# Optimization experiments

Measured on AMD Instinct MI355X. Metric: run time of the kernel, lower is better.

Reference implementation:

```python
import jax, jax.numpy as jnp
import numpy as np

NUM_HEADS = 12
NUM_GROUPS = 4
METRIC_SCALE = 1.0
CLS_MIX = 1.0
MEAN_MIX = 0.5
ROUTER_SCALE = 1.0
DIFF_SCALE = 1.0
B, N, D, HF = 16, 577, 768, 3072


def _ln(x, g, b, eps=1e-5):
    mu = jnp.mean(x, axis=-1, keepdims=True)
    var = jnp.mean(jnp.square(x - mu), axis=-1, keepdims=True)
    return (x - mu) * jax.lax.rsqrt(var + eps) * g + b


def setup_inputs() -> dict:
    key = jax.random.key(0)
    ks = iter(jax.random.split(key, 16))
    w = lambda shape, std: jax.random.normal(next(ks), shape, jnp.float32) * std
    return {
        "x": w((B, N, D), 1.0),
        "ln1_g": jnp.ones((D,)), "ln1_b": jnp.zeros((D,)),
        "ad_ln_g": jnp.ones((D,)), "ad_ln_b": jnp.zeros((D,)),
        "ad_w": w((D, D), 0.02),
        "w_qkv": w((D, 3 * D), 0.02),
        "w_proj": w((D, D), 0.02), "b_proj": jnp.zeros((D,)),
        "ln2_g": jnp.ones((D,)), "ln2_b": jnp.zeros((D,)),
        "fc1_w": w((D, HF), 0.02), "fc1_b": jnp.zeros((HF,)),
        "fc2_w": w((HF, D), 0.02), "fc2_b": jnp.zeros((D,)),
        "r_ln_g": jnp.ones((HF,)), "r_ln_b": jnp.zeros((HF,)),
        "r_proj_w": w((2 * HF, NUM_GROUPS), 0.02), "r_proj_b": jnp.zeros((NUM_GROUPS,)),
        "r_gate_w": w((2 * HF, 1), 0.02), "r_gate_b": jnp.full((1,), -2.0),
        "r_scale": jnp.full((NUM_GROUPS,), 0.1),
        "d_ln_g": jnp.ones((HF,)), "d_ln_b": jnp.zeros((HF,)),
        "d_out_w": w((HF, HF), 0.005),
        "d_gate_w": w((HF, 1), 0.02), "d_gate_b": jnp.full((1,), -1.5),
    }


def reference(x, ln1_g, ln1_b, ad_ln_g, ad_ln_b, ad_w, w_qkv, w_proj, b_proj,
              ln2_g, ln2_b, fc1_w, fc1_b, fc2_w, fc2_b,
              r_ln_g, r_ln_b, r_proj_w, r_proj_b, r_gate_w, r_gate_b, r_scale,
              d_ln_g, d_ln_b, d_out_w, d_gate_w, d_gate_b):
    b, n, d = x.shape
    hd = d // NUM_HEADS
    # ---- GeoAttention (pre-norm) ----
    h = _ln(x, ln1_g, ln1_b)
    # metric adapter: residual LN+Linear (SharedAttentionMetricAdapter)
    metric_h = h + METRIC_SCALE * (_ln(h, ad_ln_g, ad_ln_b) @ ad_w)
    # q,k from metric path; v from plain path (asymmetric Q/K vs V)
    qk = metric_h @ w_qkv[:, : 2 * d]                # [b,n,2d]
    v = h @ w_qkv[:, 2 * d :]                        # [b,n,d]
    q = qk[..., :d].reshape(b, n, NUM_HEADS, hd).transpose(0, 2, 1, 3)
    k = qk[..., d:].reshape(b, n, NUM_HEADS, hd).transpose(0, 2, 1, 3)
    v = v.reshape(b, n, NUM_HEADS, hd).transpose(0, 2, 1, 3)
    attn = jax.nn.softmax(jnp.einsum("bhnd,bhmd->bhnm", q, k) * (hd ** -0.5), axis=-1)
    out = jnp.einsum("bhnm,bhmd->bhnd", attn, v).transpose(0, 2, 1, 3).reshape(b, n, d)
    x = x + out @ w_proj + b_proj
    # ---- GeoMlp (pre-norm) ----
    h2 = _ln(x, ln2_g, ln2_b)
    hid = h2 @ fc1_w + fc1_b                         # [b,n,HF]
    # GroupCompetitionRouter on hidden
    rn = _ln(hid, r_ln_g, r_ln_b)
    summary = jnp.concatenate([CLS_MIX * rn[:, 0], MEAN_MIX * jnp.mean(rn[:, 1:], axis=1)], axis=-1)  # [b,2HF]
    wts = jax.nn.softmax(summary @ r_proj_w + r_proj_b, axis=-1)       # [b,G]
    gate = jax.nn.sigmoid(summary @ r_gate_w + r_gate_b)               # [b,1]
    centered = wts * float(NUM_GROUPS) - 1.0
    grouped = hid.reshape(b, n, NUM_GROUPS, HF // NUM_GROUPS)
    scale = 1.0 + ROUTER_SCALE * gate[:, None, :, None] * r_scale[None, None, :, None] * centered[:, None, :, None]
    hid = (grouped * scale).reshape(b, n, HF)
    # TokenDiffusionMixer on hidden
    dn = _ln(hid, d_ln_g, d_ln_b)
    tr = dn / jnp.maximum(jnp.linalg.norm(dn, axis=-1, keepdims=True), 1e-12)
    aff = jax.nn.softmax(jnp.einsum("bnc,bmc->bnm", tr, tr) * (HF ** -0.5), axis=-1)
    diffusion = jnp.einsum("bnm,bmc->bnc", aff, dn) - dn
    dgate = jax.nn.sigmoid(dn[:, 0] @ d_gate_w + d_gate_b)             # [b,1]
    hid = hid + DIFF_SCALE * dgate[:, :, None] * (diffusion @ d_out_w)
    # activation + fc2
    hid = jax.nn.gelu(hid, approximate=False)
    return x + hid @ fc2_w + fc2_b
```

## Files before the change

kernel.cpp:

```cpp
#include <hip/hip_runtime.h>
#include <math.h>

typedef unsigned short u16;
typedef unsigned int   u32;
typedef __attribute__((ext_vector_type(4))) float f32x4;
typedef __attribute__((ext_vector_type(4))) u32   u32x4;

#define DEV __device__ __forceinline__
#define AS1 __attribute__((address_space(1)))
#define AS3 __attribute__((address_space(3)))

DEV float b2f(u16 u){ u32 x = ((u32)u)<<16; float f; __builtin_memcpy(&f,&x,4); return f; }
DEV u16 f2b(float f){ u32 x; __builtin_memcpy(&x,&f,4); u32 r = x + 0x7FFFu + ((x>>16)&1u); return (u16)(r>>16); }

DEV float ldf(const float* p, long i){ return p[i]; }
DEV float ldf(const u16*   p, long i){ return b2f(p[i]); }

DEV void gload16(const u16* g, u16* l){
  __builtin_amdgcn_global_load_lds((const AS1 u32*)(const void*)g,
                                   (AS3 u32*)(void*)l, 16, 0, 0);
}

DEV float wave_sum(float v){
#pragma unroll
  for(int o=32;o;o>>=1) v += __shfl_down(v,o,64);
  return v;
}
DEV float wave_max(float v){
#pragma unroll
  for(int o=32;o;o>>=1) v = fmaxf(v, __shfl_down(v,o,64));
  return v;
}
DEV float block_sum(float v, float* tmp){
  v = wave_sum(v);
  if((threadIdx.x&63)==0) tmp[threadIdx.x>>6]=v;
  __syncthreads();
  float r = tmp[0]+tmp[1]+tmp[2]+tmp[3];
  __syncthreads();
  return r;
}
DEV float block_max(float v, float* tmp){
  v = wave_max(v);
  if((threadIdx.x&63)==0) tmp[threadIdx.x>>6]=v;
  __syncthreads();
  float r = fmaxf(fmaxf(tmp[0],tmp[1]),fmaxf(tmp[2],tmp[3]));
  __syncthreads();
  return r;
}

template<typename TI>
__global__ void transpose_pad(const TI* __restrict__ in, u16* __restrict__ out,
                              int R, int C, int Rpad, long strideI, long strideO){
  __shared__ u16 t[32][33];
  in  += (long)blockIdx.z*strideI;
  out += (long)blockIdx.z*strideO;
  int tx = threadIdx.x & 31, ty = threadIdx.x >> 5;
  int bc = blockIdx.x*32, br = blockIdx.y*32;
#pragma unroll
  for(int i=0;i<32;i+=8){
    int r = br+ty+i, c = bc+tx;
    float v = (r<R && c<C) ? ldf(in,(long)r*C+c) : 0.f;
    t[ty+i][tx] = f2b(v);
  }
  __syncthreads();
#pragma unroll
  for(int i=0;i<32;i+=8){
    int c = bc+ty+i, r = br+tx;
    if(c<C && r<Rpad) out[(long)c*Rpad + r] = t[tx][ty+i];
  }
}

template<typename TI>
__global__ void ln_rows(const TI* __restrict__ x, const float* __restrict__ g,
                        const float* __restrict__ b, u16* __restrict__ y, int W){
  __shared__ float tmp[4];
  long base=(long)blockIdx.x*W;
  float s=0.f, ss=0.f;
  for(int c=threadIdx.x;c<W;c+=256){ float v=ldf(x,base+c); s+=v; ss+=v*v; }
  s=block_sum(s,tmp); ss=block_sum(ss,tmp);
  float mu=s/W;
  float rstd=rsqrtf(fmaxf(ss/W-mu*mu,0.f)+1e-5f);
  for(int c=threadIdx.x;c<W;c+=256){
    float v=ldf(x,base+c);
    y[base+c]=f2b((v-mu)*rstd*g[c]+b[c]);
  }
}

__global__ void row_stats(const u16* __restrict__ x, float* __restrict__ stats, int W){
  __shared__ float tmp[4];
  long base=(long)blockIdx.x*W;
  float s=0.f,ss=0.f;
  for(int c=threadIdx.x;c<W;c+=256){ float v=b2f(x[base+c]); s+=v; ss+=v*v; }
  s=block_sum(s,tmp); ss=block_sum(ss,tmp);
  if(threadIdx.x==0){
    float mu=s/W;
    stats[2*(long)blockIdx.x]=mu;
    stats[2*(long)blockIdx.x+1]=rsqrtf(fmaxf(ss/W-mu*mu,0.f)+1e-5f);
  }
}

__global__ void dn_kernel(const u16* __restrict__ x, const float* __restrict__ g,
                          const float* __restrict__ b, const float* __restrict__ scalef,
                          u16* __restrict__ dn, float* __restrict__ rn){
  const int W=3072;
  __shared__ float tmp[4];
  __shared__ u16 rowb[3072];
  long row=(long)blockIdx.x;
  long base=row*(long)W;
  int bz=(int)(row/577);
  float s=0.f,ss=0.f;
  for(int c=threadIdx.x;c<W;c+=256){
    float sc=scalef[bz*4 + ((c>>8)/3)];
    float v=b2f(x[base+c])*sc;
    rowb[c]=f2b(v);
    s+=v; ss+=v*v;
  }
  s=block_sum(s,tmp); ss=block_sum(ss,tmp);
  float mu=s/W;
  float rstd=rsqrtf(fmaxf(ss/W-mu*mu,0.f)+1e-5f);
  float sq=0.f;
  for(int c=threadIdx.x;c<W;c+=256){
    float v=(b2f(rowb[c])-mu)*rstd*g[c]+b[c];
    sq+=v*v;
  }
  sq=block_sum(sq,tmp);
  float r=1.f/fmaxf(sqrtf(sq),1e-12f);
  for(int c=threadIdx.x;c<W;c+=256){
    float v=(b2f(rowb[c])-mu)*rstd*g[c]+b[c];
    dn[base+c]=f2b(v);
  }
  if(threadIdx.x==0) rn[blockIdx.x]=r;
}

__global__ void softmax_rows(u16* __restrict__ S, int W, int Wp,
                             const float* __restrict__ rs, int rpb, float alpha){
  __shared__ float tmp[4];
  long row = blockIdx.x;
  u16* p = S + row*(long)Wp;
  float rowscale = alpha;
  const float* rsb = nullptr;
  if(rs){ long bt=row/rpb; int m=(int)(row%rpb); rsb = rs + bt*(long)rpb; rowscale *= rsb[m]; }
  float mx=-3e38f;
  for(int c=threadIdx.x;c<W;c+=256){
    float v=b2f(p[c])*rowscale; if(rs) v*=rsb[c];
    mx=fmaxf(mx,v);
  }
  mx=block_max(mx,tmp);
  float sm=0.f;
  for(int c=threadIdx.x;c<W;c+=256){
    float v=b2f(p[c])*rowscale; if(rs) v*=rsb[c];
    sm+=__expf(v-mx);
  }
  sm=block_sum(sm,tmp);
  float inv=1.f/sm;
  for(int c=threadIdx.x;c<W;c+=256){
    float v=b2f(p[c])*rowscale; if(rs) v*=rsb[c];
    p[c]=f2b(__expf(v-mx)*inv);
  }
  for(int c=W+threadIdx.x;c<Wp;c+=256) p[c]=0;
}

__global__ void split_heads(const u16* __restrict__ qk, u16* __restrict__ qh, u16* __restrict__ kh){
  int i = blockIdx.x*256+threadIdx.x;
  if(i >= 16*577*12*8) return;
  int dv = i&7; int h=(i>>3)%12; int bn=i/96;
  int b=bn/577, n=bn%577;
  long src=(long)bn*1536 + h*64 + dv*8;
  long dst=((long)((b*12+h)*577+n))*64 + dv*8;
  *(u32x4*)(qh+dst) = *(const u32x4*)(qk+src);
  *(u32x4*)(kh+dst) = *(const u32x4*)(qk+src+768);
}
__global__ void merge_heads(const u16* __restrict__ aoh, u16* __restrict__ aout){
  int i = blockIdx.x*256+threadIdx.x;
  if(i >= 16*577*12*8) return;
  int dv=i&7; int h=(i>>3)%12; int bn=i/96;
  int b=bn/577, n=bn%577;
  long dst=(long)bn*768 + h*64 + dv*8;
  long src=((long)((b*12+h)*577+n))*64 + dv*8;
  *(u32x4*)(aout+dst) = *(const u32x4*)(aoh+src);
}
__global__ void make_vT(const u16* __restrict__ v, u16* __restrict__ vT){
  long i = (long)blockIdx.x*256+threadIdx.x;
  if(i >= (long)192*64*608) return;
  int n=(int)(i%608); long q=i/608; int d=(int)(q&63); int bh=(int)(q>>6);
  int b=bh/12, h=bh%12;
  u16 val=0;
  if(n<577) val = v[((long)(b*577+n))*768 + h*64 + d];
  vT[i]=val;
}

__global__ void summary_kernel(const u16* __restrict__ hid, const float* __restrict__ stats,
                               const float* __restrict__ rg, const float* __restrict__ rb,
                               float* __restrict__ summ){
  int b=blockIdx.y;
  int c=blockIdx.x*256+threadIdx.x;
  const u16* hb=hid+(size_t)b*577*3072;
  const float* st=stats+(size_t)b*577*2;
  float g=rg[c], be=rb[c];
  float cls=(b2f(hb[c])-st[0])*st[1]*g+be;
  float acc=0.f;
  for(int n=1;n<577;n++) acc += (b2f(hb[(size_t)n*3072+c])-st[2*n])*st[2*n+1];
  summ[(size_t)b*6144+c]        = 1.0f*cls;
  summ[(size_t)b*6144+3072+c]   = 0.5f*(g*(acc*(1.f/576.f))+be);
}

__global__ void router_kernel(const float* __restrict__ summ, const float* __restrict__ pw,
                              const float* __restrict__ pb, const float* __restrict__ gw,
                              const float* __restrict__ gb, const float* __restrict__ rsc,
                              float* __restrict__ scalef){
  __shared__ float tmp[4];
  int b=blockIdx.x;
  float a0=0,a1=0,a2=0,a3=0,a4=0;
  for(int c=threadIdx.x;c<6144;c+=256){
    float sv=summ[(size_t)b*6144+c];
    a0+=sv*pw[c*4+0]; a1+=sv*pw[c*4+1]; a2+=sv*pw[c*4+2]; a3+=sv*pw[c*4+3];
    a4+=sv*gw[c];
  }
  a0=block_sum(a0,tmp); a1=block_sum(a1,tmp); a2=block_sum(a2,tmp);
  a3=block_sum(a3,tmp); a4=block_sum(a4,tmp);
  if(threadIdx.x==0){
    float l0=a0+pb[0], l1=a1+pb[1], l2=a2+pb[2], l3=a3+pb[3];
    float mx=fmaxf(fmaxf(l0,l1),fmaxf(l2,l3));
    float e0=__expf(l0-mx),e1=__expf(l1-mx),e2=__expf(l2-mx),e3=__expf(l3-mx);
    float s=e0+e1+e2+e3;
    float gate=1.f/(1.f+__expf(-(a4+gb[0])));
    float w0=e0/s,w1=e1/s,w2=e2/s,w3=e3/s;
    scalef[b*4+0]=1.f+gate*rsc[0]*(4.f*w0-1.f);
    scalef[b*4+1]=1.f+gate*rsc[1]*(4.f*w1-1.f);
    scalef[b*4+2]=1.f+gate*rsc[2]*(4.f*w2-1.f);
    scalef[b*4+3]=1.f+gate*rsc[3]*(4.f*w3-1.f);
  }
}

__global__ void dgate_kernel(const u16* __restrict__ dn, const float* __restrict__ gw,
                             const float* __restrict__ gb, float* __restrict__ dgate){
  __shared__ float tmp[4];
  int b=blockIdx.x;
  const u16* row = dn + (size_t)b*577*3072;
  float a=0.f;
  for(int c=threadIdx.x;c<3072;c+=256) a+=b2f(row[c])*gw[c];
  a=block_sum(a,tmp);
  if(threadIdx.x==0) dgate[b]=1.f/(1.f+__expf(-(a+gb[0])));
}

constexpr int F_BIAS=1, F_RES=2, F_GELU=4, F_GATE=8, F_RESF32=16, F_OUTF32=32, F_SCRES=64;

DEV int swz(int u){ int row=u>>2, sl=u&3; return row*4 + (sl ^ ((row>>1)&3)); }

template<int FLAGS>
__global__ __launch_bounds__(256,2) void gemm_bt(
  const u16* __restrict__ A, long lda, long szA,
  const u16* __restrict__ B, long ldb, long szB,
  void* __restrict__ Cv, long ldc, long szC,
  const float* __restrict__ bias,
  const void* __restrict__ resv, long ldr, long szR, float res_scale,
  const float* __restrict__ gate,
  float alpha, int M, int N, int K, int NX, int NY)
{
  __shared__ alignas(16) u16 shA[128*32];
  __shared__ alignas(16) u16 shB[128*32];
  const int nwg = (int)gridDim.x;
  const int orig = (int)blockIdx.x;
  const int q = nwg>>3, r = nwg&7;
  const int xcd = orig&7, idx = orig>>3;
  const int wg = (xcd<r ? xcd*(q+1) : r*(q+1)+(xcd-r)*q) + idx;
  const int bx = wg % NX; const int t_ = wg / NX;
  const int by = t_ % NY; const int z  = t_ / NY;

  A += (long)z*szA; B += (long)z*szB;
  const int tid=threadIdx.x, lane=tid&63, wid=tid>>6;
  const int wr=wid>>1, wc=wid&1;
  const long m0=(long)bx*128, n0=(long)by*128;
  f32x4 acc[4][4];
#pragma unroll
  for(int i=0;i<4;i++)
#pragma unroll
    for(int j=0;j<4;j++){ f32x4 zv={0.f,0.f,0.f,0.f}; acc[i][j]=zv; }

  const int lr = lane>>2, lsl = lane&3;
  const u16* pA[2]; const u16* pB[2]; u16* lA[2]; u16* lB[2];
#pragma unroll
  for(int i=0;i<2;i++){
    int ra = wid*32 + i*16 + lr;
    int kc = (lsl ^ ((ra>>1)&3))*8;
    long gr = m0+ra; if(gr>=M) gr=M-1;
    long gb = n0+ra; if(gb>=N) gb=N-1;
    pA[i] = A + gr*lda + kc;
    pB[i] = B + gb*ldb + kc;
    lA[i] = shA + (wid*32 + i*16)*32;
    lB[i] = shB + (wid*32 + i*16)*32;
  }

  for(int k0=0;k0<K;k0+=32){
    __syncthreads();
#pragma unroll
    for(int i=0;i<2;i++){
      gload16(pA[i]+k0, lA[i]);
      gload16(pB[i]+k0, lB[i]);
    }
    __syncthreads();
    const int ks = lane>>4, rr = lane&15;
    u32x4 av[4], bv[4];
#pragma unroll
    for(int mi=0;mi<4;mi++) av[mi] = ((const u32x4*)shA)[swz((wr*64+mi*16+rr)*4+ks)];
#pragma unroll
    for(int ni=0;ni<4;ni++) bv[ni] = ((const u32x4*)shB)[swz((wc*64+ni*16+rr)*4+ks)];
#pragma unroll
    for(int mi=0;mi<4;mi++)
#pragma unroll
      for(int ni=0;ni<4;ni++)
        asm volatile("v_mfma_f32_16x16x32_bf16 %0, %1, %2, %0"
                     : "+v"(acc[mi][ni]) : "v"(av[mi]), "v"(bv[ni]));
  }
  const float* resf = (const float*)resv + (long)z*szR;
  const u16*   resh = (const u16*)resv   + (long)z*szR;
  float* Cf = (float*)Cv + (long)z*szC;
  u16*   Ch = (u16*)Cv   + (long)z*szC;
  float gv = (FLAGS&F_GATE)? gate[z] : 1.f;
#pragma unroll
  for(int mi=0;mi<4;mi++){
#pragma unroll
    for(int ni=0;ni<4;ni++){
      long c0 = n0 + wc*64 + ni*16 + (lane&15);
      if(c0>=N) continue;
      float bb = (FLAGS&F_BIAS)? bias[c0] : 0.f;
#pragma unroll
      for(int r2=0;r2<4;r2++){
        long rw = m0 + wr*64 + mi*16 + (lane>>4)*4 + r2;
        if(rw>=M) continue;
        float t = acc[mi][ni][r2]*alpha*gv + bb;
        if(FLAGS&F_RES){
          float rvv = (FLAGS&F_RESF32)? resf[rw*ldr+c0] : b2f(resh[rw*ldr+c0]);
          t += res_scale*rvv;
        }
        if(FLAGS&F_GELU) t = 0.5f*t*(1.f+erff(t*0.70710678118654752f));
        if(FLAGS&F_OUTF32) Cf[rw*ldc+c0]=t;
        else               Ch[rw*ldc+c0]=f2b(t);
      }
    }
  }
}

static inline int gpack(int M,int N,int nb,int& NX,int& NY){
  NX=(M+127)/128; NY=(N+127)/128; return NX*NY*nb;
}

template<int FLAGS>
__global__ __launch_bounds__(512,2) void gemm256(
  const u16* __restrict__ A, long lda,
  const u16* __restrict__ B, long ldb,
  u16* __restrict__ C, long ldc,
  const float* __restrict__ bias,
  const u16* __restrict__ res, long ldr,
  const float* __restrict__ gate, const float* __restrict__ scres,
  float irpz, float alpha, int M, int N, int K, int NX)
{
  __shared__ u16 smem[65536];
  const int nwg=(int)gridDim.x, orig=(int)blockIdx.x;
  const int qq=nwg>>3, rr8=nwg&7, xcd=orig&7, idx=orig>>3;
  const int wg=(xcd<rr8? xcd*(qq+1): rr8*(qq+1)+(xcd-rr8)*qq)+idx;
  const int bx=wg%NX, by=wg/NX;
  const long m0=(long)bx*256, n0=(long)by*256;
  const int tid=threadIdx.x, lane=tid&63, wid=tid>>6;
  const int wr=wid>>2, wc=wid&3;

  f32x4 acc[8][4];
#pragma unroll
  for(int i=0;i<8;i++)
#pragma unroll
    for(int j=0;j<4;j++){ f32x4 zv={0.f,0.f,0.f,0.f}; acc[i][j]=zv; }

  const u16* sA[2][2]; const u16* sB[2][2];
#pragma unroll
  for(int kh=0;kh<2;kh++)
#pragma unroll
    for(int jj=0;jj<2;jj++){
      int s=jj*512+tid, row=s>>2, sl=(s&3)^((s>>3)&3);
      long ar=m0+row; if(ar>=M) ar=M-1;
      long br=n0+row; if(br>=N) br=N-1;
      sA[kh][jj]=A+ar*lda+kh*32+sl*8;
      sB[kh][jj]=B+br*ldb+kh*32+sl*8;
    }
  const int dst0=(wid*64)*8, dst1=(512+wid*64)*8;
  const int ks=lane>>4, l15=lane&15;
  const int phys=(ks^((l15>>1)&3))*8;
  const int aBase=(wr*128+l15)*32+phys;
  const int bBase=(wc*64 +l15)*32+phys;
  const int NT=K>>6;

#define STG(t,c,kh) { long k0_=(long)(t)*64; \
    gload16(sA[kh][0]+k0_, smem + (c)*16384 + (kh)*8192 + dst0); \
    gload16(sA[kh][1]+k0_, smem + (c)*16384 + (kh)*8192 + dst1); \
    gload16(sB[kh][0]+k0_, smem + 32768 + (c)*16384 + (kh)*8192 + dst0); \
    gload16(sB[kh][1]+k0_, smem + 32768 + (c)*16384 + (kh)*8192 + dst1); }

  STG(0,0,0); STG(0,0,1);
  asm volatile("s_waitcnt vmcnt(4)" ::: "memory");
  __builtin_amdgcn_s_barrier();
  asm volatile("" ::: "memory");

  u32x4 av[4], bv[4];
  for(int t=0;t<NT;++t){
    const int cur=t&1, nxt=cur^1;
    const u16* sa=smem + cur*16384;
    const u16* sb=smem + 32768 + cur*16384;
    const bool pf=(t+1<NT);
    if(pf) STG(t+1,nxt,0);
#pragma unroll
    for(int j=0;j<4;j++) bv[j]=*(const u32x4*)(sb + bBase + j*512);
#pragma unroll
    for(int i=0;i<4;i++) av[i]=*(const u32x4*)(sa + aBase + i*512);
    __builtin_amdgcn_s_setprio(1);
#pragma unroll
    for(int i=0;i<4;i++)
#pragma unroll
      for(int j=0;j<4;j++)
        asm volatile("v_mfma_f32_16x16x32_bf16 %0, %1, %2, %0":"+v"(acc[i][j]):"v"(av[i]),"v"(bv[j]));
    __builtin_amdgcn_s_setprio(0);
#pragma unroll
    for(int i=0;i<4;i++) av[i]=*(const u32x4*)(sa + aBase + 2048 + i*512);
    __builtin_amdgcn_s_setprio(1);
#pragma unroll
    for(int i=0;i<4;i++)
#pragma unroll
      for(int j=0;j<4;j++)
        asm volatile("v_mfma_f32_16x16x32_bf16 %0, %1, %2, %0":"+v"(acc[4+i][j]):"v"(av[i]),"v"(bv[j]));
    __builtin_amdgcn_s_setprio(0);
    if(pf) asm volatile("s_waitcnt vmcnt(4)" ::: "memory");
    else   asm volatile("s_waitcnt vmcnt(0)" ::: "memory");
    __builtin_amdgcn_s_barrier();
    asm volatile("" ::: "memory");
    if(pf) STG(t+1,nxt,1);
#pragma unroll
    for(int j=0;j<4;j++) bv[j]=*(const u32x4*)(sb + 8192 + bBase + j*512);
#pragma unroll
    for(int i=0;i<4;i++) av[i]=*(const u32x4*)(sa + 8192 + aBase + i*512);
    __builtin_amdgcn_s_setprio(1);
#pragma unroll
    for(int i=0;i<4;i++)
#pragma unroll
      for(int j=0;j<4;j++)
        asm volatile("v_mfma_f32_16x16x32_bf16 %0, %1, %2, %0":"+v"(acc[i][j]):"v"(av[i]),"v"(bv[j]));
    __builtin_amdgcn_s_setprio(0);
#pragma unroll
    for(int i=0;i<4;i++) av[i]=*(const u32x4*)(sa + 8192 + aBase + 2048 + i*512);
    __builtin_amdgcn_s_setprio(1);
#pragma unroll
    for(int i=0;i<4;i++)
#pragma unroll
      for(int j=0;j<4;j++)
        asm volatile("v_mfma_f32_16x16x32_bf16 %0, %1, %2, %0":"+v"(acc[4+i][j]):"v"(av[i]),"v"(bv[j]));
    __builtin_amdgcn_s_setprio(0);
    if(pf) asm volatile("s_waitcnt vmcnt(4)" ::: "memory");
    else   asm volatile("s_waitcnt vmcnt(0)" ::: "memory");
    __builtin_amdgcn_s_barrier();
    asm volatile("" ::: "memory");
  }
#undef STG

#pragma unroll
  for(int mf=0;mf<8;mf++){
#pragma unroll
    for(int j=0;j<4;j++){
      long c0 = n0 + wc*64 + j*16 + l15;
      float bb=(FLAGS&F_BIAS)? bias[c0]:0.f;
      int cg=((int)(c0>>8))/3;
#pragma unroll
      for(int r2=0;r2<4;r2++){
        long rw = m0 + wr*128 + mf*16 + ks*4 + r2;
        if(rw>=M) continue;
        float t=acc[mf][j][r2]*alpha;
        if(FLAGS&(F_GATE|F_SCRES)){
          int z=(int)(((float)rw+0.5f)*irpz);
          if(FLAGS&F_GATE) t*=gate[z];
          if(FLAGS&F_SCRES) t += scres[z*4+cg]*b2f(res[rw*ldr+c0]);
        } else if(FLAGS&F_RES){
          t += b2f(res[rw*ldr+c0]);
        }
        t+=bb;
        if(FLAGS&F_GELU) t=0.5f*t*(1.f+erff(t*0.70710678118654752f));
        C[rw*ldc+c0]=f2b(t);
      }
    }
  }
}

extern "C" void kernel_launch(void* const* d_in, const int* in_sizes, int n_in,
                              void* d_out, int out_size, void* d_ws, size_t ws_size,
                              hipStream_t stream){
  const int BNr=16*577;
  const float* x      = (const float*)d_in[0];
  const float* ln1_g  = (const float*)d_in[1];
  const float* ln1_b  = (const float*)d_in[2];
  const float* ad_ln_g= (const float*)d_in[3];
  const float* ad_ln_b= (const float*)d_in[4];
  const float* ad_w   = (const float*)d_in[5];
  const float* w_qkv  = (const float*)d_in[6];
  const float* w_proj = (const float*)d_in[7];
  const float* b_proj = (const float*)d_in[8];
  const float* ln2_g  = (const float*)d_in[9];
  const float* ln2_b  = (const float*)d_in[10];
  const float* fc1_w  = (const float*)d_in[11];
  const float* fc1_b  = (const float*)d_in[12];
  const float* fc2_w  = (const float*)d_in[13];
  const float* fc2_b  = (const float*)d_in[14];
  const float* r_ln_g = (const float*)d_in[15];
  const float* r_ln_b = (const float*)d_in[16];
  const float* r_proj_w=(const float*)d_in[17];
  const float* r_proj_b=(const float*)d_in[18];
  const float* r_gate_w=(const float*)d_in[19];
  const float* r_gate_b=(const float*)d_in[20];
  const float* r_scale =(const float*)d_in[21];
  const float* d_ln_g = (const float*)d_in[22];
  const float* d_ln_b = (const float*)d_in[23];
  const float* d_outw = (const float*)d_in[24];
  const float* d_gate_w=(const float*)d_in[25];
  const float* d_gate_b=(const float*)d_in[26];

  char* ws=(char*)d_ws;
  size_t off=0;
  auto take=[&](size_t nb){ size_t r=off; off=(off+nb+255)&~(size_t)255; return r; };
  auto al  =[&](size_t v){ return (v+255)&~(size_t)255; };
  const size_t o_qkvT = take((size_t)2304*768*2);
  const size_t o_adT  = take((size_t)768*768*2);
  const size_t o_projT= take((size_t)768*768*2);
  const size_t o_fc1T = take((size_t)3072*768*2);
  const size_t o_fc2T = take((size_t)768*3072*2);
  const size_t o_doutT= take((size_t)3072*3072*2);
  const size_t o_x2   = take((size_t)BNr*768*4);
  const size_t o_hid  = take((size_t)BNr*3072*2);
  const size_t o_stats= take((size_t)BNr*2*4);
  const size_t o_rn   = take((size_t)BNr*4);
  const size_t o_sum  = take((size_t)16*6144*4);
  const size_t o_scalef=take(64*4);
  const size_t o_dg   = take(64);
  const size_t o_h    = take((size_t)BNr*768*2);
  const size_t o_lnh  = take((size_t)BNr*768*2);
  const size_t o_metric=take((size_t)BNr*768*2);
  const size_t o_qk   = take((size_t)BNr*1536*2);
  const size_t o_v    = take((size_t)BNr*768*2);
  const size_t o_qh   = take((size_t)192*577*64*2);
  const size_t o_kh   = take((size_t)192*577*64*2);
  const size_t o_vT   = take((size_t)192*64*608*2);
  (void)o_v; (void)o_vT; (void)ws_size; (void)in_sizes; (void)n_in; (void)out_size;
  const size_t o_S    = o_qk;
  const size_t o_aoh  = o_metric;
  const size_t o_aout = o_h;
  const size_t o_h2   = o_lnh;
  const size_t o_dn   = o_h;
  const size_t o_aff  = al(o_dn + (size_t)BNr*3072*2);
  const size_t o_dnTb = al(o_aff + (size_t)16*577*608*2);
  const size_t o_diff = al(o_dnTb + (size_t)4*3072*608*2);
  const size_t o_hact = o_dn;

  u16* qkvT=(u16*)(ws+o_qkvT); u16* adT=(u16*)(ws+o_adT); u16* projT=(u16*)(ws+o_projT);
  u16* fc1T=(u16*)(ws+o_fc1T); u16* fc2T=(u16*)(ws+o_fc2T); u16* doutT=(u16*)(ws+o_doutT);
  float* x2=(float*)(ws+o_x2); u16* hid=(u16*)(ws+o_hid);
  float* stats=(float*)(ws+o_stats); float* rn=(float*)(ws+o_rn);
  float* summ=(float*)(ws+o_sum); float* scalef=(float*)(ws+o_scalef); float* dgate=(float*)(ws+o_dg);
  u16* hbuf=(u16*)(ws+o_h); u16* lnh=(u16*)(ws+o_lnh); u16* metric=(u16*)(ws+o_metric);
  u16* qkbuf=(u16*)(ws+o_qk); u16* vbuf=(u16*)(ws+o_v);
  u16* qh=(u16*)(ws+o_qh); u16* kh=(u16*)(ws+o_kh); u16* vT=(u16*)(ws+o_vT);
  u16* Sc=(u16*)(ws+o_S); u16* aoh=(u16*)(ws+o_aoh); u16* aout=(u16*)(ws+o_aout);
  u16* h2=(u16*)(ws+o_h2);
  u16* dn=(u16*)(ws+o_dn); u16* aff=(u16*)(ws+o_aff); u16* dnTb=(u16*)(ws+o_dnTb);
  u16* diff=(u16*)(ws+o_diff); u16* hact=(u16*)(ws+o_hact);

  dim3 blk(256), blk5(512);
  int NX, NY, ng;
  transpose_pad<float><<<dim3(72,24,1),blk,0,stream>>>(w_qkv, qkvT, 768,2304,768, 0,0);
  transpose_pad<float><<<dim3(24,24,1),blk,0,stream>>>(ad_w,  adT,  768,768, 768, 0,0);
  transpose_pad<float><<<dim3(24,24,1),blk,0,stream>>>(w_proj,projT,768,768, 768, 0,0);
  transpose_pad<float><<<dim3(96,24,1),blk,0,stream>>>(fc1_w, fc1T, 768,3072,768, 0,0);
  transpose_pad<float><<<dim3(24,96,1),blk,0,stream>>>(fc2_w, fc2T, 3072,768,3072,0,0);
  transpose_pad<float><<<dim3(96,96,1),blk,0,stream>>>(d_outw,doutT,3072,3072,3072,0,0);
  ln_rows<float><<<BNr,blk,0,stream>>>(x, ln1_g, ln1_b, hbuf, 768);
  ln_rows<u16>  <<<BNr,blk,0,stream>>>(hbuf, ad_ln_g, ad_ln_b, lnh, 768);
  ng=gpack(BNr,768,1,NX,NY);
  gemm_bt<F_RES><<<ng,blk,0,stream>>>(lnh,768,0, adT,768,0, metric,768,0,
      nullptr, hbuf,768,0, 1.f, nullptr, 1.f, BNr,768,768, NX,NY);
  gemm256<0><<<dim3(37*6),blk5,0,stream>>>(metric,768, qkvT,768, qkbuf,1536,
      nullptr, nullptr,0, nullptr,nullptr, 0.f, 1.f, BNr,1536,768, 37);
  ng=gpack(BNr,768,1,NX,NY);
  gemm_bt<0><<<ng,blk,0,stream>>>(hbuf,768,0, qkvT+(size_t)1536*768,768,0, vbuf,768,0,
      nullptr, nullptr,0,0,0.f, nullptr, 1.f, BNr,768,768, NX,NY);
  split_heads<<<3462,blk,0,stream>>>(qkbuf, qh, kh);
  make_vT<<<29184,blk,0,stream>>>(vbuf, vT);
  for(int c=0;c<6;c++){
    const u16* qc=qh+(size_t)c*32*577*64;
    const u16* kc=kh+(size_t)c*32*577*64;
    ng=gpack(577,577,32,NX,NY);
    gemm_bt<0><<<ng,blk,0,stream>>>(qc,64,(long)577*64, kc,64,(long)577*64,
        Sc,608,(long)577*608, nullptr, nullptr,0,0,0.f, nullptr, 0.125f, 577,577,64, NX,NY);
    softmax_rows<<<32*577,blk,0,stream>>>(Sc,577,608, nullptr,577, 1.f);
    ng=gpack(577,64,32,NX,NY);
    gemm_bt<0><<<ng,blk,0,stream>>>(Sc,608,(long)577*608, vT+(size_t)c*32*64*608,608,(long)64*608,
        aoh+(size_t)c*32*577*64,64,(long)577*64, nullptr, nullptr,0,0,0.f, nullptr, 1.f, 577,64,608, NX,NY);
  }
  merge_heads<<<3462,blk,0,stream>>>(aoh, aout);
  ng=gpack(BNr,768,1,NX,NY);
  gemm_bt<F_RES|F_BIAS|F_RESF32|F_OUTF32><<<ng,blk,0,stream>>>(aout,768,0, projT,768,0,
      x2,768,0, b_proj, x,768,0, 1.f, nullptr, 1.f, BNr,768,768, NX,NY);
  ln_rows<float><<<BNr,blk,0,stream>>>(x2, ln2_g, ln2_b, h2, 768);
  gemm256<F_BIAS><<<dim3(37*12),blk5,0,stream>>>(h2,768, fc1T,768, hid,3072,
      fc1_b, nullptr,0, nullptr,nullptr, 0.f, 1.f, BNr,3072,768, 37);
  row_stats<<<BNr,blk,0,stream>>>(hid, stats, 3072);
  summary_kernel<<<dim3(12,16),blk,0,stream>>>(hid, stats, r_ln_g, r_ln_b, summ);
  router_kernel<<<16,blk,0,stream>>>(summ, r_proj_w, r_proj_b, r_gate_w, r_gate_b, r_scale, scalef);
  dn_kernel<<<BNr,blk,0,stream>>>(hid, d_ln_g, d_ln_b, scalef, dn, rn);
  dgate_kernel<<<16,blk,0,stream>>>(dn, d_gate_w, d_gate_b, dgate);
  ng=gpack(577,577,16,NX,NY);
  gemm_bt<0><<<ng,blk,0,stream>>>(dn,3072,(long)577*3072, dn,3072,(long)577*3072,
      aff,608,(long)577*608, nullptr, nullptr,0,0,0.f, nullptr, 1.f, 577,577,3072, NX,NY);
  softmax_rows<<<BNr,blk,0,stream>>>(aff,577,608, rn,577, 0.01804219634f);
  for(int g4=0; g4<4; ++g4){
    transpose_pad<u16><<<dim3(96,19,4),blk,0,stream>>>(dn+(size_t)g4*4*577*3072, dnTb,
        577,3072,608, (long)577*3072, (long)3072*608);
    ng=gpack(577,3072,4,NX,NY);
    gemm_bt<F_RES><<<ng,blk,0,stream>>>(aff+(size_t)g4*4*577*608,608,(long)577*608,
        dnTb,608,(long)3072*608, diff+(size_t)g4*4*577*3072,3072,(long)577*3072,
        nullptr, dn+(size_t)g4*4*577*3072,3072,(long)577*3072, -1.f, nullptr, 1.f, 577,3072,608, NX,NY);
  }
  gemm256<F_GELU|F_GATE|F_SCRES><<<dim3(37*12),blk5,0,stream>>>(diff,3072, doutT,3072,
      hact,3072, nullptr, hid,3072, dgate, scalef, 1.f/577.f, 1.f, BNr,3072,3072, 37);
  ng=gpack(BNr,768,1,NX,NY);
  gemm_bt<F_RES|F_BIAS|F_RESF32|F_OUTF32><<<ng,blk,0,stream>>>(hact,3072,0,
      fc2T,3072,0, d_out,768,0, fc2_b, x2,768,0, 1.f, nullptr, 1.f, BNr,768,3072, NX,NY);
}
```

Measured before the change: 1.522 ms.

## Restructure gemm256 mainloop into 8-phase pipeline with full-K tile layout

Rewrites the main loop of the 256x256 GEMM kernel. Each buffer now holds a full 64-wide K slice per row with an XOR swizzle, where before it was split into two 32-wide halves. Global-to-LDS prefetch runs two tiles ahead and is split into four staggered quarter-loads interleaved between MFMA groups, with barriers around each MFMA cluster. The intent is to overlap LDS and global loads with MFMA work more evenly and to reduce bank conflicts. The cost is more barriers per iteration and tighter vmcnt accounting that could be fragile.

```diff
diff --git a/kernel.cpp b/kernel.cpp
--- a/kernel.cpp
+++ b/kernel.cpp
@@ -355,14 +355,15 @@
   const float* __restrict__ gate, const float* __restrict__ scres,
   float irpz, float alpha, int M, int N, int K, int NX)
 {
-  __shared__ u16 smem[65536];
+  __shared__ alignas(16) u16 smem[65536];
+  char* sm=(char*)smem;
   const int nwg=(int)gridDim.x, orig=(int)blockIdx.x;
   const int qq=nwg>>3, rr8=nwg&7, xcd=orig&7, idx=orig>>3;
   const int wg=(xcd<rr8? xcd*(qq+1): rr8*(qq+1)+(xcd-rr8)*qq)+idx;
   const int bx=wg%NX, by=wg/NX;
   const long m0=(long)bx*256, n0=(long)by*256;
   const int tid=threadIdx.x, lane=tid&63, wid=tid>>6;
-  const int wr=wid>>2, wc=wid&3;
+  const int wr=wid>>2, wc=wid&3, l15=lane&15, ks=lane>>4;
 
   f32x4 acc[8][4];
 #pragma unroll
@@ -370,93 +371,84 @@
 #pragma unroll
     for(int j=0;j<4;j++){ f32x4 zv={0.f,0.f,0.f,0.f}; acc[i][j]=zv; }
 
-  const u16* sA[2][2]; const u16* sB[2][2];
-#pragma unroll
-  for(int kh=0;kh<2;kh++)
-#pragma unroll
-    for(int jj=0;jj<2;jj++){
-      int s=jj*512+tid, row=s>>2, sl=(s&3)^((s>>3)&3);
-      long ar=m0+row; if(ar>=M) ar=M-1;
-      long br=n0+row; if(br>=N) br=N-1;
-      sA[kh][jj]=A+ar*lda+kh*32+sl*8;
-      sB[kh][jj]=B+br*ldb+kh*32+sl*8;
+  const u16 *sA[2][2], *sB[2][2];
+  int dstj[2];
+#pragma unroll
+  for(int j=0;j<2;j++){
+    int u=j*512+tid, row=u>>3;
+    long co=(long)(((u&7)^(row&7))*8);
+    dstj[j]=u*16;
+#pragma unroll
+    for(int h=0;h<2;h++){
+      long gr=m0+h*128+row; if(gr>=M) gr=M-1;
+      long gb=n0+h*128+row; if(gb>=N) gb=N-1;
+      sA[h][j]=A+gr*lda+co;
+      sB[h][j]=B+gb*ldb+co;
     }
-  const int dst0=(wid*64)*8, dst1=(512+wid*64)*8;
-  const int ks=lane>>4, l15=lane&15;
-  const int phys=(ks^((l15>>1)&3))*8;
-  const int aBase=(wr*128+l15)*32+phys;
-  const int bBase=(wc*64 +l15)*32+phys;
+  }
+  int xsl[2]; xsl[0]=((ks^(l15&7))<<4); xsl[1]=(((4+ks)^(l15&7))<<4);
+  const int arow = wr*16384 + l15*128;
+  int brow[4];
+#pragma unroll
+  for(int nj=0;nj<4;nj++){ int n=wc*64+nj*16; brow[nj]=32768+(n>>7)*16384+((n&127)+l15)*128; }
   const int NT=K>>6;
 
-#define STG(t,c,kh) { long k0_=(long)(t)*64; \
-    gload16(sA[kh][0]+k0_, smem + (c)*16384 + (kh)*8192 + dst0); \
-    gload16(sA[kh][1]+k0_, smem + (c)*16384 + (kh)*8192 + dst1); \
-    gload16(sB[kh][0]+k0_, smem + 32768 + (c)*16384 + (kh)*8192 + dst0); \
-    gload16(sB[kh][1]+k0_, smem + 32768 + (c)*16384 + (kh)*8192 + dst1); }
-
-  STG(0,0,0); STG(0,0,1);
-  asm volatile("s_waitcnt vmcnt(4)" ::: "memory");
-  __builtin_amdgcn_s_barrier();
-  asm volatile("" ::: "memory");
-
-  u32x4 av[4], bv[4];
+#define STG(P,mat,h,kt,bf) { \
+  gload16(P[h][0]+(long)(kt)*64,(u16*)(sm+(bf)*65536+(mat)*32768+(h)*16384+dstj[0])); \
+  gload16(P[h][1]+(long)(kt)*64,(u16*)(sm+(bf)*65536+(mat)*32768+(h)*16384+dstj[1])); }
+#define BAR() { asm volatile("":::"memory"); __builtin_amdgcn_s_barrier(); asm volatile("":::"memory"); }
+#define MFMA16(A0,KB) { \
+  __builtin_amdgcn_s_setprio(1); \
+  _Pragma("unroll") for(int i_=0;i_<4;i_++) \
+  _Pragma("unroll") for(int j_=0;j_<4;j_++) \
+    asm volatile("v_mfma_f32_16x16x32_bf16 %0, %1, %2, %0" \
+                 :"+v"(acc[(A0)+i_][j_]):"v"(av[i_]),"v"(bv[KB][j_])); \
+  __builtin_amdgcn_s_setprio(0); }
+
+  STG(sB,1,0,0,0); STG(sB,1,1,0,0); STG(sA,0,0,0,0); STG(sA,0,1,0,0);
+  if(NT>1){ STG(sB,1,0,1,1); STG(sB,1,1,1,1); STG(sA,0,0,1,1); }
+  if(NT>1) asm volatile("s_waitcnt vmcnt(6)":::"memory");
+  else     asm volatile("s_waitcnt vmcnt(0)":::"memory");
+  BAR();
+
+  u32x4 av[4], bv[2][4];
   for(int t=0;t<NT;++t){
     const int cur=t&1, nxt=cur^1;
-    const u16* sa=smem + cur*16384;
-    const u16* sb=smem + 32768 + cur*16384;
-    const bool pf=(t+1<NT);
-    if(pf) STG(t+1,nxt,0);
-#pragma unroll
-    for(int j=0;j<4;j++) bv[j]=*(const u32x4*)(sb + bBase + j*512);
-#pragma unroll
-    for(int i=0;i<4;i++) av[i]=*(const u32x4*)(sa + aBase + i*512);
-    __builtin_amdgcn_s_setprio(1);
-#pragma unroll
-    for(int i=0;i<4;i++)
-#pragma unroll
-      for(int j=0;j<4;j++)
-        asm volatile("v_mfma_f32_16x16x32_bf16 %0, %1, %2, %0":"+v"(acc[i][j]):"v"(av[i]),"v"(bv[j]));
-    __builtin_amdgcn_s_setprio(0);
-#pragma unroll
-    for(int i=0;i<4;i++) av[i]=*(const u32x4*)(sa + aBase + 2048 + i*512);
-    __builtin_amdgcn_s_setprio(1);
-#pragma unroll
-    for(int i=0;i<4;i++)
-#pragma unroll
-      for(int j=0;j<4;j++)
-        asm volatile("v_mfma_f32_16x16x32_bf16 %0, %1, %2, %0":"+v"(acc[4+i][j]):"v"(av[i]),"v"(bv[j]));
-    __builtin_amdgcn_s_setprio(0);
-    if(pf) asm volatile("s_waitcnt vmcnt(4)" ::: "memory");
-    else   asm volatile("s_waitcnt vmcnt(0)" ::: "memory");
-    __builtin_amdgcn_s_barrier();
-    asm volatile("" ::: "memory");
-    if(pf) STG(t+1,nxt,1);
-#pragma unroll
-    for(int j=0;j<4;j++) bv[j]=*(const u32x4*)(sb + 8192 + bBase + j*512);
-#pragma unroll
-    for(int i=0;i<4;i++) av[i]=*(const u32x4*)(sa + 8192 + aBase + i*512);
-    __builtin_amdgcn_s_setprio(1);
-#pragma unroll
-    for(int i=0;i<4;i++)
-#pragma unroll
-      for(int j=0;j<4;j++)
-        asm volatile("v_mfma_f32_16x16x32_bf16 %0, %1, %2, %0":"+v"(acc[i][j]):"v"(av[i]),"v"(bv[j]));
-    __builtin_amdgcn_s_setprio(0);
-#pragma unroll
-    for(int i=0;i<4;i++) av[i]=*(const u32x4*)(sa + 8192 + aBase + 2048 + i*512);
-    __builtin_amdgcn_s_setprio(1);
-#pragma unroll
-    for(int i=0;i<4;i++)
-#pragma unroll
-      for(int j=0;j<4;j++)
-        asm volatile("v_mfma_f32_16x16x32_bf16 %0, %1, %2, %0":"+v"(acc[4+i][j]):"v"(av[i]),"v"(bv[j]));
-    __builtin_amdgcn_s_setprio(0);
-    if(pf) asm volatile("s_waitcnt vmcnt(4)" ::: "memory");
-    else   asm volatile("s_waitcnt vmcnt(0)" ::: "memory");
-    __builtin_amdgcn_s_barrier();
-    asm volatile("" ::: "memory");
+    const char* bp = sm + cur*65536;
+    if(t+1<NT) STG(sA,0,1,t+1,nxt);
+#pragma unroll
+    for(int kk=0;kk<2;kk++)
+#pragma unroll
+      for(int nj=0;nj<4;nj++) bv[kk][nj]=*(const u32x4*)(bp+brow[nj]+xsl[kk]);
+#pragma unroll
+    for(int i=0;i<4;i++) av[i]=*(const u32x4*)(bp+arow+i*2048+xsl[0]);
+    BAR();
+    MFMA16(0,0);
+    BAR();
+    if(t+2<NT) STG(sB,1,0,t+2,cur);
+#pragma unroll
+    for(int i=0;i<4;i++) av[i]=*(const u32x4*)(bp+arow+(4+i)*2048+xsl[0]);
+    BAR();
+    MFMA16(4,0);
+    BAR();
+    if(t+2<NT) STG(sB,1,1,t+2,cur);
+#pragma unroll
+    for(int i=0;i<4;i++) av[i]=*(const u32x4*)(bp+arow+i*2048+xsl[1]);
+    BAR();
+    MFMA16(0,1);
+    BAR();
+    if(t+2<NT) STG(sA,0,0,t+2,cur);
+#pragma unroll
+    for(int i=0;i<4;i++) av[i]=*(const u32x4*)(bp+arow+(4+i)*2048+xsl[1]);
+    if(t+2<NT) asm volatile("s_waitcnt vmcnt(6)":::"memory");
+    else       asm volatile("s_waitcnt vmcnt(0)":::"memory");
+    BAR();
+    MFMA16(4,1);
+    BAR();
   }
 #undef STG
+#undef BAR
+#undef MFMA16
 
 #pragma unroll
   for(int mf=0;mf<8;mf++){
```

Result: no change. 1.509 ms (-0.9%).
